# Optimization experiments

Measured on AMD Instinct MI355X. Metric: run time of the kernel, lower is better.

The kernel has to match this reference:

```python
import jax, jax.numpy as jnp
import numpy as np

NEG_SLOPE = 0.2

def _segment_softmax(logits, seg, num_segments):
    m = jax.ops.segment_max(logits, seg, num_segments=num_segments)
    m = jnp.where(jnp.isfinite(m), m, 0.0)
    e = jnp.exp(logits - m[seg])
    s = jax.ops.segment_sum(e, seg, num_segments=num_segments)
    return e / (s[seg] + 1e-16)

def _gat_conv(x, src, dst, W, att_src, att_dst, b):
    # PyG GATConv, heads=1, concat=True, add_self_loops=True
    N = x.shape[0]
    h = x @ W                                   # [N, C]
    a_src = h @ att_src                         # [N]
    a_dst = h @ att_dst                         # [N]
    loop = jnp.arange(N, dtype=src.dtype)
    s = jnp.concatenate([src, loop])            # add self-loops
    d = jnp.concatenate([dst, loop])
    logits = jax.nn.leaky_relu(a_src[s] + a_dst[d], NEG_SLOPE)  # [E+N]
    w = _segment_softmax(logits, d, N)
    out = jax.ops.segment_sum(h[s] * w[:, None], d, num_segments=N)
    return out + b

def _sage_conv(x, src, dst, W_l, W_r, b):
    # PyG SAGEConv, aggr='mean', root_weight=True, normalize=False
    N = x.shape[0]
    agg = jax.ops.segment_sum(x[src], dst, num_segments=N)      # [N, C]
    deg = jax.ops.segment_sum(jnp.ones_like(src, dtype=x.dtype), dst, num_segments=N)
    mean = agg / jnp.maximum(deg, 1.0)[:, None]
    return mean @ W_l + x @ W_r + b

def setup_inputs() -> dict:
    key = jax.random.key(0)
    ks = jax.random.split(key, 12)
    N, E, EL, F_IN, D = 100000, 1000000, 200000, 11, 64
    glorot = lambda k, sh: jax.random.uniform(k, sh, jnp.float32, -1.0, 1.0) * np.sqrt(6.0 / (sh[0] + sh[-1]))
    return {
        "x": jax.random.normal(ks[0], (N, F_IN), jnp.float32),
        "edge_index": jax.random.randint(ks[1], (2, E), 0, N, jnp.int64),
        "edge_label_index": jax.random.randint(ks[2], (2, EL), 0, N, jnp.int64),
        "W_gat": glorot(ks[3], (F_IN, D)),
        "att_src": glorot(ks[4], (D,)),
        "att_dst": glorot(ks[5], (D,)),
        "b_gat": jnp.zeros((D,), jnp.float32),
        "W1_l": glorot(ks[6], (D, D)),
        "W1_r": glorot(ks[7], (D, D)),
        "b1": jnp.zeros((D,), jnp.float32),
        "W2_l": glorot(ks[8], (D, D)),
        "W2_r": glorot(ks[9], (D, D)),
        "b2": jnp.zeros((D,), jnp.float32),
        "alpha": jnp.full((4,), 1.0 / 4.0, jnp.float32),  # num_layers + 1
    }

def reference(x, edge_index, edge_label_index, W_gat, att_src, att_dst, b_gat,
              W1_l, W1_r, b1, W2_l, W2_r, b2, alpha):
    src, dst = edge_index[0], edge_index[1]
    weights = jax.nn.softmax(alpha)
    # Faithful to original get_embedding (note: weights[1] is skipped, as in source)
    h = _gat_conv(x, src, dst, W_gat, att_src, att_dst, b_gat)
    out = h * weights[0]
    h = _sage_conv(h, src, dst, W1_l, W1_r, b1)
    out = out + h * weights[2]
    h = _sage_conv(h, src, dst, W2_l, W2_r, b2)
    out = out + h * weights[3]
    # link prediction: gather + elementwise dot
    return (out[edge_label_index[0]] * out[edge_label_index[1]]).sum(-1)
```

## Files before the change

kernel.cpp:

```cpp
#include <hip/hip_runtime.h>
#include <math.h>
#include <float.h>

#define NEG_SLOPE 0.2f
#define NCHUNK 128

typedef _Float16 half8 __attribute__((ext_vector_type(8)));
typedef float f32x4  __attribute__((ext_vector_type(4)));

__global__ __launch_bounds__(256) void gat_input_kernel(
    const float* __restrict__ x, const float* __restrict__ Wg,
    const float* __restrict__ att_src, const float* __restrict__ att_dst,
    _Float16* __restrict__ Hf, float* __restrict__ a_src, float* __restrict__ a_dst, int N,
    const float* __restrict__ W1l, const float* __restrict__ W1r,
    const float* __restrict__ W2l, const float* __restrict__ W2r,
    _Float16* __restrict__ W1hi, _Float16* __restrict__ W1lo,
    _Float16* __restrict__ W2hi, _Float16* __restrict__ W2lo,
    const float* __restrict__ alpha, float* __restrict__ wsm,
    _Float16* __restrict__ HG, _Float16* __restrict__ H1)
{
    if (blockIdx.x < 8) {
        if (blockIdx.x == 0 && threadIdx.x == 0) {
            float m = alpha[0];
            for (int i = 1; i < 4; i++) m = fmaxf(m, alpha[i]);
            float e[4], s = 0.f;
            for (int i = 0; i < 4; i++) { e[i] = expf(alpha[i] - m); s += e[i]; }
            for (int i = 0; i < 4; i++) wsm[i] = e[i] / s;
        }
        int which = blockIdx.x >> 2;
        const float* Wl = which ? W2l : W1l;
        const float* Wr = which ? W2r : W1r;
        _Float16* Whi = which ? W2hi : W1hi;
        _Float16* Wlo = which ? W2lo : W1lo;
        int idx = (blockIdx.x & 3) * 256 + threadIdx.x;
        int kc = idx >> 8, rem = idx & 255;
        int t = rem >> 6, ln = rem & 63;
        int quad = ln >> 4, col16 = ln & 15;
        int c = t * 16 + col16;
        #pragma unroll
        for (int j = 0; j < 8; j++) {
            int k = kc * 32 + quad * 8 + j;
            float w = (k < 64) ? Wl[k * 64 + c] : Wr[(k - 64) * 64 + c];
            _Float16 hi = (_Float16)w;
            _Float16 lo = (_Float16)(w - (float)hi);
            Whi[(size_t)idx * 8 + j] = hi;
            Wlo[(size_t)idx * 8 + j] = lo;
        }
    } else if (blockIdx.x == 8) {
        if (threadIdx.x < 64) Hf[(size_t)N * 64 + threadIdx.x] = (_Float16)0.f;
        else if (threadIdx.x < 128) HG[(size_t)N * 64 + (threadIdx.x - 64)] = (_Float16)0.f;
        else if (threadIdx.x < 192) H1[(size_t)N * 64 + (threadIdx.x - 128)] = (_Float16)0.f;
        else if (threadIdx.x == 192) a_src[N] = -1e30f;
    }
    __shared__ float Wl[11 * 64];
    int tid = threadIdx.x;
    for (int i = tid; i < 11 * 64; i += 256) Wl[i] = Wg[i];
    __syncthreads();
    int lane = tid & 63;
    int n = blockIdx.x * 4 + (tid >> 6);
    if (n >= N) return;
    float xv = (lane < 11) ? x[n * 11 + lane] : 0.f;
    float acc = 0.f;
    #pragma unroll
    for (int k = 0; k < 11; k++) acc += __shfl(xv, k, 64) * Wl[k * 64 + lane];
    Hf[(size_t)n * 64 + lane] = (_Float16)acc;
    float ps = acc * att_src[lane];
    float pd = acc * att_dst[lane];
    for (int off = 32; off; off >>= 1) {
        ps += __shfl_down(ps, off, 64);
        pd += __shfl_down(pd, off, 64);
    }
    if (lane == 0) { a_src[n] = ps; a_dst[n] = pd; }
}


__global__ __launch_bounds__(1024) void edge_hist_kernel(
    const int* __restrict__ dst, int* __restrict__ hist, int E, int NBK)
{
    __shared__ int c[1024];
    int t = threadIdx.x;
    c[t] = 0;
    __syncthreads();
    int chunk = (E + NCHUNK - 1) / NCHUNK;
    int lo = blockIdx.x * chunk;
    int hi = lo + chunk; if (hi > E) hi = E;
    for (int i = lo + t; i < hi; i += 1024)
        atomicAdd(&c[dst[i] >> 7], 1);
    __syncthreads();
    if (t < NBK) hist[t * NCHUNK + blockIdx.x] = c[t];
}

__global__ __launch_bounds__(1024) void edge_scatter_kernel(
    const int* __restrict__ src, const int* __restrict__ dst,
    const int* __restrict__ rstart, unsigned* __restrict__ ebuf, int E, int NBK)
{
    __shared__ int cur[1024];
    int t = threadIdx.x;
    if (t < NBK) cur[t] = rstart[t * NCHUNK + blockIdx.x];
    __syncthreads();
    int chunk = (E + NCHUNK - 1) / NCHUNK;
    int lo = blockIdx.x * chunk;
    int hi = lo + chunk; if (hi > E) hi = E;
    for (int i = lo + t; i < hi; i += 1024) {
        int d = dst[i];
        int p = atomicAdd(&cur[d >> 7], 1);
        ebuf[p] = ((unsigned)src[i] << 7) | (unsigned)(d & 127);
    }
}

__global__ __launch_bounds__(256) void scan_reduce_kernel(
    const int* __restrict__ v, int* __restrict__ bsum, int M)
{
    __shared__ int s[256];
    int t = threadIdx.x;
    int base = blockIdx.x * 1024 + t * 4;
    int sum = 0;
    #pragma unroll
    for (int j = 0; j < 4; j++) { int idx = base + j; if (idx < M) sum += v[idx]; }
    s[t] = sum; __syncthreads();
    for (int off = 128; off; off >>= 1) {
        if (t < off) s[t] += s[t + off];
        __syncthreads();
    }
    if (t == 0) bsum[blockIdx.x] = s[0];
}

__global__ __launch_bounds__(256) void scan_apply_kernel(
    const int* __restrict__ v, const int* __restrict__ bsum,
    int* __restrict__ out, int M, int NB)
{
    __shared__ int s[256];
    int t = threadIdx.x;
    int bv = (t < NB) ? bsum[t] : 0;
    s[t] = bv; __syncthreads();
    for (int off = 1; off < 256; off <<= 1) {
        int xx = (t >= off) ? s[t - off] : 0;
        __syncthreads();
        s[t] += xx;
        __syncthreads();
    }
    int blockoff = (blockIdx.x == 0) ? 0 : s[blockIdx.x - 1];
    __syncthreads();
    int base = blockIdx.x * 1024;
    int vv[4]; int sum = 0;
    #pragma unroll
    for (int j = 0; j < 4; j++) {
        int idx = base + t * 4 + j;
        vv[j] = (idx < M) ? v[idx] : 0;
        sum += vv[j];
    }
    s[t] = sum; __syncthreads();
    for (int off = 1; off < 256; off <<= 1) {
        int xx = (t >= off) ? s[t - off] : 0;
        __syncthreads();
        s[t] += xx;
        __syncthreads();
    }
    int ex = s[t] - sum + blockoff;
    #pragma unroll
    for (int j = 0; j < 4; j++) {
        int idx = base + t * 4 + j;
        if (idx < M) out[idx] = ex;
        ex += vv[j];
    }
}

__global__ __launch_bounds__(256) void bucket_build_kernel(
    const unsigned* __restrict__ ebuf, const int* __restrict__ rstart,
    int* __restrict__ cnt, int* __restrict__ rowstart,
    int* __restrict__ csr, int E, int N, int NBK)
{
    __shared__ int c[128];
    __shared__ int rs[128];
    __shared__ int cur[128];
    int b = blockIdx.x, t = threadIdx.x;
    if (t < 128) { c[t] = 0; cur[t] = 0; }
    __syncthreads();
    int beg = rstart[b * NCHUNK];
    int end = (b == NBK - 1) ? E : rstart[(b + 1) * NCHUNK];
    int n = end - beg;
    int pbeg = beg + 384 * b;
    for (int j = t; j < n; j += 256)
        atomicAdd(&c[ebuf[beg + j] & 127u], 1);
    __syncthreads();
    int myc = (t < 128) ? c[t] : 0;
    int mypc = (myc + 3) & ~3;
    if (t < 128) rs[t] = mypc;
    __syncthreads();
    for (int off = 1; off < 128; off <<= 1) {
        int v = (t < 128 && t >= off) ? rs[t - off] : 0;
        __syncthreads();
        if (t < 128) rs[t] += v;
        __syncthreads();
    }
    int ex = (t < 128) ? (rs[t] - mypc) : 0;
    __syncthreads();
    if (t < 128) rs[t] = ex;
    int base = b << 7;
    if (t < 128 && base + t < N) {
        cnt[base + t] = myc;
        rowstart[base + t] = pbeg + ex;
    }
    __syncthreads();
    for (int j = t; j < n; j += 256) {
        unsigned e = ebuf[beg + j];
        int d = (int)(e & 127u);
        int p = atomicAdd(&cur[d], 1);
        csr[pbeg + rs[d] + p] = (int)(e >> 7);
    }
    __syncthreads();
    if (t < 128) {
        for (int k = myc; k < mypc; k++) csr[pbeg + rs[t] + k] = N;
    }
}

__global__ __launch_bounds__(256) void gat_gather_kernel(
    const _Float16* __restrict__ Hf, const float* __restrict__ a_src,
    const float* __restrict__ a_dst, const float* __restrict__ bg,
    const int* __restrict__ rowstart, const int* __restrict__ cnt,
    const int* __restrict__ csr, const float* __restrict__ wsm,
    _Float16* __restrict__ HG, _Float16* __restrict__ outD, int N)
{
    const half8* __restrict__ H8 = (const half8*)Hf;
    int tid = threadIdx.x;
    int lane = tid & 63;
    int g = lane >> 3, sub = lane & 7;
    int gl = g << 3;
    int d = blockIdx.x * 32 + (tid >> 3);
    if (d >= N) return;
    float ad = a_dst[d];
    int beg = rowstart[d], deg = cnt[d];
    int degp = (deg + 3) & ~3;
    float a0 = a_src[d] + ad;
    float lg0 = a0 > 0.f ? a0 : NEG_SLOPE * a0;
    float w_self = expf(lg0);
    half8 hself = H8[(size_t)d * 8 + sub];
    float acc[8];
    #pragma unroll
    for (int c = 0; c < 8; c++) acc[c] = w_self * (float)hself[c];
    float l_lane = 0.f;
    for (int base = 0; base < degp; base += 8) {
        int nvc = degp - base; if (nvc > 8) nvc = 8;
        int sid = (sub < nvc) ? csr[beg + base + sub] : N;
        float aa = a_src[sid] + ad;
        float lgt = aa > 0.f ? aa : NEG_SLOPE * aa;
        float w = expf(lgt);
        l_lane += w;
        int ib[8]; float wb[8];
        #pragma unroll
        for (int j = 0; j < 8; j++) {
            ib[j] = __shfl(sid, gl + j, 64);
            wb[j] = __shfl(w, gl + j, 64);
        }
        half8 v[8];
        #pragma unroll
        for (int j = 0; j < 8; j++) v[j] = H8[(size_t)ib[j] * 8 + sub];
        #pragma unroll
        for (int j = 0; j < 8; j++) {
            #pragma unroll
            for (int c = 0; c < 8; c++) acc[c] += wb[j] * (float)v[j][c];
        }
    }
    #pragma unroll
    for (int off = 1; off < 8; off <<= 1) l_lane += __shfl_xor(l_lane, off, 64);
    float l = l_lane + w_self;
    float inv = 1.0f / (l + 1e-16f);
    float w0s = wsm[0];
    size_t idx = (size_t)d * 8 + sub;
    half8 hg, od;
    #pragma unroll
    for (int c = 0; c < 8; c++) {
        float o = acc[c] * inv + bg[sub * 8 + c];
        hg[c] = (_Float16)o;
        od[c] = (_Float16)(w0s * o);
    }
    ((half8*)HG)[idx] = hg;
    ((half8*)outD)[idx] = od;
}

__global__ __launch_bounds__(256) void sage_fused_kernel(
    const _Float16* __restrict__ Hin,
    const _Float16* __restrict__ Whi, const _Float16* __restrict__ Wlo,
    const float* __restrict__ bvec,
    const int* __restrict__ rowstart, const int* __restrict__ cnt,
    const int* __restrict__ csr, const float* __restrict__ wsm, int widx,
    _Float16* __restrict__ hout, _Float16* __restrict__ outD, int N)
{
    __shared__ __align__(16) char smem[64 * 68 * 4];
    float* Ot = (float*)smem;
    const half8* __restrict__ H8 = (const half8*)Hin;
    int tid = threadIdx.x;
    int lane = tid & 63;
    int nodeBase = blockIdx.x * 64;
    int sub = tid & 7;
    int g = lane >> 3;
    int gl = g << 3;

    #pragma unroll
    for (int pass = 0; pass < 2; pass++) {
        int dloc = pass * 32 + (tid >> 3);
        int d = nodeBase + dloc;
        float acc[8];
        #pragma unroll
        for (int c = 0; c < 8; c++) acc[c] = 0.f;
        half8 hself;
        #pragma unroll
        for (int c = 0; c < 8; c++) hself[c] = (_Float16)0.f;
        float invd = 0.f;
        if (d < N) {
            int beg = rowstart[d], deg = cnt[d];
            int degp = (deg + 3) & ~3;
            for (int base2 = 0; base2 < degp; base2 += 8) {
                int nvc = degp - base2; if (nvc > 8) nvc = 8;
                int sid = (sub < nvc) ? csr[beg + base2 + sub] : N;
                int ib[8];
                #pragma unroll
                for (int j = 0; j < 8; j++) ib[j] = __shfl(sid, gl + j, 64);
                half8 v[8];
                #pragma unroll
                for (int j = 0; j < 8; j++) v[j] = H8[(size_t)ib[j] * 8 + sub];
                #pragma unroll
                for (int j = 0; j < 8; j++) {
                    #pragma unroll
                    for (int c = 0; c < 8; c++) acc[c] += (float)v[j][c];
                }
            }
            invd = 1.0f / fmaxf((float)deg, 1.0f);
            hself = H8[(size_t)d * 8 + sub];
        }
        half8 ah;
        #pragma unroll
        for (int c = 0; c < 8; c++) ah[c] = (_Float16)(acc[c] * invd);
        int rbase = dloc * 256;
        int swz = (dloc & 7) << 4;
        *(half8*)(smem + ((rbase + sub * 16) ^ swz)) = ah;
        *(half8*)(smem + ((rbase + 128 + sub * 16) ^ swz)) = hself;
    }
    __syncthreads();

    int quad = lane >> 4, col16 = lane & 15;
    int wave = tid >> 6;
    int row = wave * 16 + col16;
    int rswz = (row & 7) << 4;
    f32x4 accq[4];
    #pragma unroll
    for (int t = 0; t < 4; t++) accq[t] = (f32x4){0.f, 0.f, 0.f, 0.f};
    #pragma unroll
    for (int kc = 0; kc < 4; kc++) {
        half8 a = *(const half8*)(smem + ((row * 256 + kc * 64 + quad * 16) ^ rswz));
        #pragma unroll
        for (int t = 0; t < 4; t++) {
            size_t off = (size_t)((kc * 4 + t) * 64 + lane) * 8;
            half8 bhi = *(const half8*)(Whi + off);
            half8 blo = *(const half8*)(Wlo + off);
            accq[t] = __builtin_amdgcn_mfma_f32_16x16x32_f16(a, bhi, accq[t], 0, 0, 0);
            accq[t] = __builtin_amdgcn_mfma_f32_16x16x32_f16(a, blo, accq[t], 0, 0, 0);
        }
    }
    __syncthreads();
    #pragma unroll
    for (int t = 0; t < 4; t++) {
        #pragma unroll
        for (int r = 0; r < 4; r++) {
            Ot[(wave * 16 + quad * 4 + r) * 68 + t * 16 + col16] = accq[t][r];
        }
    }
    __syncthreads();

    float w = wsm[widx];
    #pragma unroll
    for (int pass = 0; pass < 2; pass++) {
        int dloc = pass * 32 + (tid >> 3);
        int d = nodeBase + dloc;
        if (d >= N) continue;
        size_t idx = (size_t)d * 8 + sub;
        float4 o0 = *(float4*)&Ot[dloc * 68 + sub * 8];
        float4 o1 = *(float4*)&Ot[dloc * 68 + sub * 8 + 4];
        float4 b0 = *(const float4*)&bvec[sub * 8];
        float4 b1 = *(const float4*)&bvec[sub * 8 + 4];
        float o[8] = {o0.x + b0.x, o0.y + b0.y, o0.z + b0.z, o0.w + b0.w,
                      o1.x + b1.x, o1.y + b1.y, o1.z + b1.z, o1.w + b1.w};
        half8 od = ((half8*)outD)[idx];
        half8 ho;
        #pragma unroll
        for (int c = 0; c < 8; c++) {
            ho[c] = (_Float16)o[c];
            od[c] = (_Float16)((float)od[c] + w * o[c]);
        }
        if (hout) ((half8*)hout)[idx] = ho;
        ((half8*)outD)[idx] = od;
    }
}

__global__ __launch_bounds__(256) void link_pred_kernel(
    const int* __restrict__ eli, const _Float16* __restrict__ outf,
    float* __restrict__ out, int EL)
{
    const half8* __restrict__ o8 = (const half8*)outf;
    int e = blockIdx.x * 32 + (threadIdx.x >> 3);
    int sub = threadIdx.x & 7;
    if (e >= EL) return;
    int a = eli[e], b = eli[EL + e];
    half8 pa = o8[(size_t)a * 8 + sub];
    half8 pb = o8[(size_t)b * 8 + sub];
    float p = 0.f;
    #pragma unroll
    for (int c = 0; c < 8; c++) p += (float)pa[c] * (float)pb[c];
    for (int off = 4; off; off >>= 1) p += __shfl_xor(p, off, 64);
    if (sub == 0) out[e] = p;
}

extern "C" void kernel_launch(void* const* d_in, const int* in_sizes, int n_in,
                              void* d_out, int out_size, void* d_ws, size_t ws_size,
                              hipStream_t stream)
{
    const float* x      = (const float*)d_in[0];
    const int*   ei     = (const int*)d_in[1];
    const int*   eli    = (const int*)d_in[2];
    const float* Wg     = (const float*)d_in[3];
    const float* att_s  = (const float*)d_in[4];
    const float* att_d  = (const float*)d_in[5];
    const float* bg     = (const float*)d_in[6];
    const float* W1l    = (const float*)d_in[7];
    const float* W1r    = (const float*)d_in[8];
    const float* b1     = (const float*)d_in[9];
    const float* W2l    = (const float*)d_in[10];
    const float* W2r    = (const float*)d_in[11];
    const float* b2     = (const float*)d_in[12];
    const float* alpha  = (const float*)d_in[13];

    const int N  = in_sizes[0] / 11;
    const int E  = in_sizes[1] / 2;
    const int EL = in_sizes[2] / 2;
    const int NBK = (N + 127) >> 7;
    const int M   = NBK * NCHUNK;
    const int CSRSZ = E + 384 * NBK;

    const int* src = ei;
    const int* dst = ei + E;

    _Float16* Hf  = (_Float16*)d_ws;
    _Float16* HG  = Hf + (size_t)(N + 1) * 64;
    _Float16* H1  = HG + (size_t)(N + 1) * 64;
    _Float16* oD  = H1 + (size_t)(N + 1) * 64;
    _Float16* wf  = oD + (size_t)N * 64;
    _Float16* W1hi = wf;
    _Float16* W1lo = wf + 8192;
    _Float16* W2hi = wf + 16384;
    _Float16* W2lo = wf + 24576;
    float* wsm     = (float*)(wf + 32768);
    float* a_src   = wsm + 4;
    float* a_dst   = a_src + (N + 1);
    int*   cnt     = (int*)(a_dst + N);
    int*   rowstart= cnt + N;
    int*   hist    = rowstart + M ? rowstart + N : rowstart + N;
    int*   rstart  = hist + M;
    int*   bsum    = rstart + M;
    int*   csr     = bsum + 256;
    unsigned* ebuf = (unsigned*)H1;

    gat_input_kernel<<<(N + 3) / 4, 256, 0, stream>>>(x, Wg, att_s, att_d, Hf, a_src, a_dst, N,
                                                      W1l, W1r, W2l, W2r,
                                                      W1hi, W1lo, W2hi, W2lo, alpha, wsm,
                                                      HG, H1);

    edge_hist_kernel<<<NCHUNK, 1024, 0, stream>>>(dst, hist, E, NBK);
    int NB = (M + 1023) / 1024;
    scan_reduce_kernel<<<NB, 256, 0, stream>>>(hist, bsum, M);
    scan_apply_kernel<<<NB, 256, 0, stream>>>(hist, bsum, rstart, M, NB);
    edge_scatter_kernel<<<NCHUNK, 1024, 0, stream>>>(src, dst, rstart, ebuf, E, NBK);
    bucket_build_kernel<<<NBK, 256, 0, stream>>>(ebuf, rstart, cnt, rowstart, csr, E, N, NBK);

    gat_gather_kernel<<<(N + 31) / 32, 256, 0, stream>>>(Hf, a_src, a_dst, bg,
                                                         rowstart, cnt, csr, wsm, HG, oD, N);

    sage_fused_kernel<<<(N + 63) / 64, 256, 0, stream>>>(HG, W1hi, W1lo, b1,
                                                         rowstart, cnt, csr, wsm, 2, H1, oD, N);

    sage_fused_kernel<<<(N + 63) / 64, 256, 0, stream>>>(H1, W2hi, W2lo, b2,
                                                         rowstart, cnt, csr, wsm, 3, nullptr, oD, N);

    link_pred_kernel<<<(EL + 31) / 32, 256, 0, stream>>>(eli, oD, (float*)d_out, EL);
}
```

Before: 248.1 us.

## Fuse the whole GAT+SAGE pipeline into one cooperative persistent kernel

Replaces the chain of ten kernel launches with one cooperative persistent mega-kernel. Every stage (input projection, histogram, scan, scatter, bucket build, GAT gather, two SAGE layers, link prediction) runs as a grid-stride phase separated by grid.sync. The goal is to remove per-launch overhead and idle tails between small kernels. The cost is fewer blocks (bounded by occupancy, capped at 2048), smaller per-block thread counts for the histogram and scatter stages, and grid-wide barrier latency. The previous multi-kernel path remains as a fallback, and ebuf moves out of H1 into its own workspace region.

After: 260.3 us. 1.05x slower.

```diff
diff --git a/kernel.cpp b/kernel.cpp
--- a/kernel.cpp
+++ b/kernel.cpp
@@ -1,12 +1,439 @@
 #include <hip/hip_runtime.h>
+#include <hip/hip_cooperative_groups.h>
 #include <math.h>
 #include <float.h>
 
+namespace cg = cooperative_groups;
+
 #define NEG_SLOPE 0.2f
 #define NCHUNK 128
 
 typedef _Float16 half8 __attribute__((ext_vector_type(8)));
 typedef float f32x4  __attribute__((ext_vector_type(4)));
+
+struct MegaArgs {
+    const float *x, *Wg, *att_s, *att_d, *bg, *W1l, *W1r, *b1, *W2l, *W2r, *b2, *alpha;
+    const int *ei, *eli;
+    float *out;
+    _Float16 *Hf, *HG, *H1, *oD, *W1hi, *W1lo, *W2hi, *W2lo;
+    float *wsm, *a_src, *a_dst;
+    int *cnt, *rowstart, *hist, *rstart, *bsum, *csr;
+    unsigned *ebuf;
+    int N, E, EL, NBK, M, NB;
+};
+
+__device__ __forceinline__ void sage_layer_phase(
+    char* smem, const _Float16* __restrict__ Hin,
+    const _Float16* __restrict__ Whi, const _Float16* __restrict__ Wlo,
+    const float* __restrict__ bvec,
+    const int* __restrict__ rowstart, const int* __restrict__ cnt,
+    const int* __restrict__ csr, const float* __restrict__ wsm, int widx,
+    _Float16* __restrict__ hout, _Float16* __restrict__ outD, int N, int G)
+{
+    float* Ot = (float*)smem;
+    const half8* __restrict__ H8 = (const half8*)Hin;
+    int tid = threadIdx.x;
+    int lane = tid & 63;
+    int sub = tid & 7;
+    int g = lane >> 3;
+    int gl = g << 3;
+    int quad = lane >> 4, col16 = lane & 15;
+    int wave = tid >> 6;
+    int NGF = (N + 63) >> 6;
+    for (int vb = blockIdx.x; vb < NGF; vb += G) {
+        int nodeBase = vb * 64;
+        #pragma unroll
+        for (int pass = 0; pass < 2; pass++) {
+            int dloc = pass * 32 + (tid >> 3);
+            int d = nodeBase + dloc;
+            float acc[8];
+            #pragma unroll
+            for (int c = 0; c < 8; c++) acc[c] = 0.f;
+            half8 hself;
+            #pragma unroll
+            for (int c = 0; c < 8; c++) hself[c] = (_Float16)0.f;
+            float invd = 0.f;
+            if (d < N) {
+                int beg = rowstart[d], deg = cnt[d];
+                int degp = (deg + 3) & ~3;
+                for (int base2 = 0; base2 < degp; base2 += 8) {
+                    int nvc = degp - base2; if (nvc > 8) nvc = 8;
+                    int sid = (sub < nvc) ? csr[beg + base2 + sub] : N;
+                    int ib[8];
+                    #pragma unroll
+                    for (int j = 0; j < 8; j++) ib[j] = __shfl(sid, gl + j, 64);
+                    half8 v[8];
+                    #pragma unroll
+                    for (int j = 0; j < 8; j++) v[j] = H8[(size_t)ib[j] * 8 + sub];
+                    #pragma unroll
+                    for (int j = 0; j < 8; j++) {
+                        #pragma unroll
+                        for (int c = 0; c < 8; c++) acc[c] += (float)v[j][c];
+                    }
+                }
+                invd = 1.0f / fmaxf((float)deg, 1.0f);
+                hself = H8[(size_t)d * 8 + sub];
+            }
+            half8 ah;
+            #pragma unroll
+            for (int c = 0; c < 8; c++) ah[c] = (_Float16)(acc[c] * invd);
+            int rbase = dloc * 256;
+            int swz = (dloc & 7) << 4;
+            *(half8*)(smem + ((rbase + sub * 16) ^ swz)) = ah;
+            *(half8*)(smem + ((rbase + 128 + sub * 16) ^ swz)) = hself;
+        }
+        __syncthreads();
+        int row = wave * 16 + col16;
+        int rswz = (row & 7) << 4;
+        f32x4 accq[4];
+        #pragma unroll
+        for (int t = 0; t < 4; t++) accq[t] = (f32x4){0.f, 0.f, 0.f, 0.f};
+        #pragma unroll
+        for (int kc = 0; kc < 4; kc++) {
+            half8 av = *(const half8*)(smem + ((row * 256 + kc * 64 + quad * 16) ^ rswz));
+            #pragma unroll
+            for (int t = 0; t < 4; t++) {
+                size_t off = (size_t)((kc * 4 + t) * 64 + lane) * 8;
+                half8 bhi = *(const half8*)(Whi + off);
+                half8 blo = *(const half8*)(Wlo + off);
+                accq[t] = __builtin_amdgcn_mfma_f32_16x16x32_f16(av, bhi, accq[t], 0, 0, 0);
+                accq[t] = __builtin_amdgcn_mfma_f32_16x16x32_f16(av, blo, accq[t], 0, 0, 0);
+            }
+        }
+        __syncthreads();
+        #pragma unroll
+        for (int t = 0; t < 4; t++) {
+            #pragma unroll
+            for (int r = 0; r < 4; r++) {
+                Ot[(wave * 16 + quad * 4 + r) * 68 + t * 16 + col16] = accq[t][r];
+            }
+        }
+        __syncthreads();
+        float w = wsm[widx];
+        #pragma unroll
+        for (int pass = 0; pass < 2; pass++) {
+            int dloc = pass * 32 + (tid >> 3);
+            int d = nodeBase + dloc;
+            if (d < N) {
+                size_t idx = (size_t)d * 8 + sub;
+                float4 o0 = *(float4*)&Ot[dloc * 68 + sub * 8];
+                float4 o1 = *(float4*)&Ot[dloc * 68 + sub * 8 + 4];
+                float4 b0 = *(const float4*)&bvec[sub * 8];
+                float4 b1v = *(const float4*)&bvec[sub * 8 + 4];
+                float o[8] = {o0.x + b0.x, o0.y + b0.y, o0.z + b0.z, o0.w + b0.w,
+                              o1.x + b1v.x, o1.y + b1v.y, o1.z + b1v.z, o1.w + b1v.w};
+                half8 od = ((half8*)outD)[idx];
+                half8 ho;
+                #pragma unroll
+                for (int c = 0; c < 8; c++) {
+                    ho[c] = (_Float16)o[c];
+                    od[c] = (_Float16)((float)od[c] + w * o[c]);
+                }
+                if (hout) ((half8*)hout)[idx] = ho;
+                ((half8*)outD)[idx] = od;
+            }
+        }
+        __syncthreads();
+    }
+}
+
+__global__ __launch_bounds__(256) void mega_kernel(MegaArgs a)
+{
+    __shared__ __align__(16) char smem[64 * 68 * 4];
+    cg::grid_group grid = cg::this_grid();
+    const int tid = threadIdx.x;
+    const int G = (int)gridDim.x;
+    const int N = a.N, E = a.E, EL = a.EL, NBK = a.NBK, M = a.M, NB = a.NB;
+    const int* src = a.ei;
+    const int* dst = a.ei + E;
+
+    if (blockIdx.x < 8) {
+        if (blockIdx.x == 0 && tid == 0) {
+            float m = a.alpha[0];
+            for (int i = 1; i < 4; i++) m = fmaxf(m, a.alpha[i]);
+            float e[4], s = 0.f;
+            for (int i = 0; i < 4; i++) { e[i] = expf(a.alpha[i] - m); s += e[i]; }
+            for (int i = 0; i < 4; i++) a.wsm[i] = e[i] / s;
+        }
+        int which = (int)blockIdx.x >> 2;
+        const float* Wlp = which ? a.W2l : a.W1l;
+        const float* Wrp = which ? a.W2r : a.W1r;
+        _Float16* Whi = which ? a.W2hi : a.W1hi;
+        _Float16* Wlo = which ? a.W2lo : a.W1lo;
+        int idx = ((int)blockIdx.x & 3) * 256 + tid;
+        int kc = idx >> 8, rem = idx & 255;
+        int t = rem >> 6, ln = rem & 63;
+        int quad = ln >> 4, col16 = ln & 15;
+        int c = t * 16 + col16;
+        #pragma unroll
+        for (int j = 0; j < 8; j++) {
+            int k = kc * 32 + quad * 8 + j;
+            float w = (k < 64) ? Wlp[k * 64 + c] : Wrp[(k - 64) * 64 + c];
+            _Float16 hi = (_Float16)w;
+            _Float16 lo = (_Float16)(w - (float)hi);
+            Whi[(size_t)idx * 8 + j] = hi;
+            Wlo[(size_t)idx * 8 + j] = lo;
+        }
+    } else if (blockIdx.x == 8) {
+        if (tid < 64) a.Hf[(size_t)N * 64 + tid] = (_Float16)0.f;
+        else if (tid < 128) a.HG[(size_t)N * 64 + (tid - 64)] = (_Float16)0.f;
+        else if (tid < 192) a.H1[(size_t)N * 64 + (tid - 128)] = (_Float16)0.f;
+        else if (tid == 192) a.a_src[N] = -1e30f;
+    }
+    {
+        float* Wl = (float*)smem;
+        for (int i = tid; i < 11 * 64; i += 256) Wl[i] = a.Wg[i];
+        __syncthreads();
+        int lane = tid & 63, wv = tid >> 6;
+        int NG = (N + 3) >> 2;
+        for (int vb = blockIdx.x; vb < NG; vb += G) {
+            int n = vb * 4 + wv;
+            if (n < N) {
+                float xv = (lane < 11) ? a.x[n * 11 + lane] : 0.f;
+                float acc = 0.f;
+                #pragma unroll
+                for (int k = 0; k < 11; k++) acc += __shfl(xv, k, 64) * Wl[k * 64 + lane];
+                a.Hf[(size_t)n * 64 + lane] = (_Float16)acc;
+                float ps = acc * a.att_s[lane];
+                float pd = acc * a.att_d[lane];
+                for (int off = 32; off; off >>= 1) {
+                    ps += __shfl_down(ps, off, 64);
+                    pd += __shfl_down(pd, off, 64);
+                }
+                if (lane == 0) { a.a_src[n] = ps; a.a_dst[n] = pd; }
+            }
+        }
+    }
+    if ((int)blockIdx.x >= G - NCHUNK) {
+        int chunk = (int)blockIdx.x - (G - NCHUNK);
+        int* c = (int*)(smem + 4096);
+        for (int i = tid; i < 1024; i += 256) c[i] = 0;
+        __syncthreads();
+        int cs = (E + NCHUNK - 1) / NCHUNK;
+        int lo = chunk * cs;
+        int hi2 = lo + cs; if (hi2 > E) hi2 = E;
+        for (int i = lo + tid; i < hi2; i += 256)
+            atomicAdd(&c[dst[i] >> 7], 1);
+        __syncthreads();
+        for (int t = tid; t < NBK; t += 256) a.hist[t * NCHUNK + chunk] = c[t];
+    }
+    grid.sync();
+
+    {
+        int* s = (int*)smem;
+        for (int vb = blockIdx.x; vb < NB; vb += G) {
+            int base = vb * 1024 + tid * 4;
+            int sum = 0;
+            #pragma unroll
+            for (int j = 0; j < 4; j++) { int idx = base + j; if (idx < M) sum += a.hist[idx]; }
+            s[tid] = sum; __syncthreads();
+            for (int off = 128; off; off >>= 1) {
+                if (tid < off) s[tid] += s[tid + off];
+                __syncthreads();
+            }
+            if (tid == 0) a.bsum[vb] = s[0];
+            __syncthreads();
+        }
+    }
+    grid.sync();
+
+    {
+        int* s = (int*)smem;
+        for (int vb = blockIdx.x; vb < NB; vb += G) {
+            int bv = (tid < NB) ? a.bsum[tid] : 0;
+            s[tid] = bv; __syncthreads();
+            for (int off = 1; off < 256; off <<= 1) {
+                int xx = (tid >= off) ? s[tid - off] : 0;
+                __syncthreads();
+                s[tid] += xx;
+                __syncthreads();
+            }
+            int blockoff = (vb == 0) ? 0 : s[vb - 1];
+            __syncthreads();
+            int base = vb * 1024;
+            int vv[4]; int sum = 0;
+            #pragma unroll
+            for (int j = 0; j < 4; j++) {
+                int idx = base + tid * 4 + j;
+                vv[j] = (idx < M) ? a.hist[idx] : 0;
+                sum += vv[j];
+            }
+            s[tid] = sum; __syncthreads();
+            for (int off = 1; off < 256; off <<= 1) {
+                int xx = (tid >= off) ? s[tid - off] : 0;
+                __syncthreads();
+                s[tid] += xx;
+                __syncthreads();
+            }
+            int ex = s[tid] - sum + blockoff;
+            #pragma unroll
+            for (int j = 0; j < 4; j++) {
+                int idx = base + tid * 4 + j;
+                if (idx < M) a.rstart[idx] = ex;
+                ex += vv[j];
+            }
+            __syncthreads();
+        }
+    }
+    grid.sync();
+
+    {
+        int* cur = (int*)smem;
+        for (int chunk = blockIdx.x; chunk < NCHUNK; chunk += G) {
+            for (int t = tid; t < 1024; t += 256)
+                cur[t] = (t < NBK) ? a.rstart[t * NCHUNK + chunk] : 0;
+            __syncthreads();
+            int cs = (E + NCHUNK - 1) / NCHUNK;
+            int lo = chunk * cs;
+            int hi2 = lo + cs; if (hi2 > E) hi2 = E;
+            for (int i = lo + tid; i < hi2; i += 256) {
+                int d = dst[i];
+                int p = atomicAdd(&cur[d >> 7], 1);
+                a.ebuf[p] = ((unsigned)src[i] << 7) | (unsigned)(d & 127);
+            }
+            __syncthreads();
+        }
+    }
+    grid.sync();
+
+    {
+        int* c   = (int*)smem;
+        int* rs  = (int*)(smem + 512);
+        int* cur = (int*)(smem + 1024);
+        for (int b = blockIdx.x; b < NBK; b += G) {
+            if (tid < 128) { c[tid] = 0; cur[tid] = 0; }
+            __syncthreads();
+            int beg = a.rstart[b * NCHUNK];
+            int end = (b == NBK - 1) ? E : a.rstart[(b + 1) * NCHUNK];
+            int n = end - beg;
+            int pbeg = beg + 384 * b;
+            for (int j = tid; j < n; j += 256)
+                atomicAdd(&c[a.ebuf[beg + j] & 127u], 1);
+            __syncthreads();
+            int myc = (tid < 128) ? c[tid] : 0;
+            int mypc = (myc + 3) & ~3;
+            if (tid < 128) rs[tid] = mypc;
+            __syncthreads();
+            for (int off = 1; off < 128; off <<= 1) {
+                int v = (tid < 128 && tid >= off) ? rs[tid - off] : 0;
+                __syncthreads();
+                if (tid < 128) rs[tid] += v;
+                __syncthreads();
+            }
+            int ex = (tid < 128) ? (rs[tid] - mypc) : 0;
+            __syncthreads();
+            if (tid < 128) rs[tid] = ex;
+            int base = b << 7;
+            if (tid < 128 && base + tid < N) {
+                a.cnt[base + tid] = myc;
+                a.rowstart[base + tid] = pbeg + ex;
+            }
+            __syncthreads();
+            for (int j = tid; j < n; j += 256) {
+                unsigned e = a.ebuf[beg + j];
+                int d = (int)(e & 127u);
+                int p = atomicAdd(&cur[d], 1);
+                a.csr[pbeg + rs[d] + p] = (int)(e >> 7);
+            }
+            __syncthreads();
+            if (tid < 128) {
+                for (int k = myc; k < mypc; k++) a.csr[pbeg + rs[tid] + k] = N;
+            }
+            __syncthreads();
+        }
+    }
+    grid.sync();
+
+    {
+        const half8* __restrict__ H8 = (const half8*)a.Hf;
+        int lane = tid & 63;
+        int g = lane >> 3, sub = lane & 7;
+        int gl = g << 3;
+        int NV = (N + 31) >> 5;
+        for (int vb = blockIdx.x; vb < NV; vb += G) {
+            int d = vb * 32 + (tid >> 3);
+            if (d < N) {
+                float ad = a.a_dst[d];
+                int beg = a.rowstart[d], deg = a.cnt[d];
+                int degp = (deg + 3) & ~3;
+                float a0 = a.a_src[d] + ad;
+                float lg0 = a0 > 0.f ? a0 : NEG_SLOPE * a0;
+                float w_self = expf(lg0);
+                half8 hself = H8[(size_t)d * 8 + sub];
+                float acc[8];
+                #pragma unroll
+                for (int c = 0; c < 8; c++) acc[c] = w_self * (float)hself[c];
+                float l_lane = 0.f;
+                for (int base = 0; base < degp; base += 8) {
+                    int nvc = degp - base; if (nvc > 8) nvc = 8;
+                    int sid = (sub < nvc) ? a.csr[beg + base + sub] : N;
+                    float aa = a.a_src[sid] + ad;
+                    float lgt = aa > 0.f ? aa : NEG_SLOPE * aa;
+                    float w = expf(lgt);
+                    l_lane += w;
+                    int ib[8]; float wb[8];
+                    #pragma unroll
+                    for (int j = 0; j < 8; j++) {
+                        ib[j] = __shfl(sid, gl + j, 64);
+                        wb[j] = __shfl(w, gl + j, 64);
+                    }
+                    half8 v[8];
+                    #pragma unroll
+                    for (int j = 0; j < 8; j++) v[j] = H8[(size_t)ib[j] * 8 + sub];
+                    #pragma unroll
+                    for (int j = 0; j < 8; j++) {
+                        #pragma unroll
+                        for (int c = 0; c < 8; c++) acc[c] += wb[j] * (float)v[j][c];
+                    }
+                }
+                #pragma unroll
+                for (int off = 1; off < 8; off <<= 1) l_lane += __shfl_xor(l_lane, off, 64);
+                float l = l_lane + w_self;
+                float inv = 1.0f / (l + 1e-16f);
+                float w0s = a.wsm[0];
+                size_t idx = (size_t)d * 8 + sub;
+                half8 hg, od;
+                #pragma unroll
+                for (int c = 0; c < 8; c++) {
+                    float o = acc[c] * inv + a.bg[sub * 8 + c];
+                    hg[c] = (_Float16)o;
+                    od[c] = (_Float16)(w0s * o);
+                }
+                ((half8*)a.HG)[idx] = hg;
+                ((half8*)a.oD)[idx] = od;
+            }
+        }
+    }
+    grid.sync();
+
+    sage_layer_phase(smem, a.HG, a.W1hi, a.W1lo, a.b1,
+                     a.rowstart, a.cnt, a.csr, a.wsm, 2, a.H1, a.oD, N, G);
+    grid.sync();
+
+    sage_layer_phase(smem, a.H1, a.W2hi, a.W2lo, a.b2,
+                     a.rowstart, a.cnt, a.csr, a.wsm, 3, nullptr, a.oD, N, G);
+    grid.sync();
+
+    {
+        const half8* __restrict__ o8 = (const half8*)a.oD;
+        int NV = (EL + 31) >> 5;
+        int sub = tid & 7;
+        for (int vb = blockIdx.x; vb < NV; vb += G) {
+            int e = vb * 32 + (tid >> 3);
+            if (e < EL) {
+                int x0 = a.eli[e], x1 = a.eli[EL + e];
+                half8 pa = o8[(size_t)x0 * 8 + sub];
+                half8 pb = o8[(size_t)x1 * 8 + sub];
+                float p = 0.f;
+                #pragma unroll
+                for (int c = 0; c < 8; c++) p += (float)pa[c] * (float)pb[c];
+                for (int off = 4; off; off >>= 1) p += __shfl_xor(p, off, 64);
+                if (sub == 0) a.out[e] = p;
+            }
+        }
+    }
+}
+
 
 __global__ __launch_bounds__(256) void gat_input_kernel(
     const float* __restrict__ x, const float* __restrict__ Wg,
@@ -72,7 +499,6 @@
     }
     if (lane == 0) { a_src[n] = ps; a_dst[n] = pd; }
 }
-
 
 __global__ __launch_bounds__(1024) void edge_hist_kernel(
     const int* __restrict__ dst, int* __restrict__ hist, int E, int NBK)
@@ -287,109 +713,8 @@
     _Float16* __restrict__ hout, _Float16* __restrict__ outD, int N)
 {
     __shared__ __align__(16) char smem[64 * 68 * 4];
-    float* Ot = (float*)smem;
-    const half8* __restrict__ H8 = (const half8*)Hin;
-    int tid = threadIdx.x;
-    int lane = tid & 63;
-    int nodeBase = blockIdx.x * 64;
-    int sub = tid & 7;
-    int g = lane >> 3;
-    int gl = g << 3;
-
-    #pragma unroll
-    for (int pass = 0; pass < 2; pass++) {
-        int dloc = pass * 32 + (tid >> 3);
-        int d = nodeBase + dloc;
-        float acc[8];
-        #pragma unroll
-        for (int c = 0; c < 8; c++) acc[c] = 0.f;
-        half8 hself;
-        #pragma unroll
-        for (int c = 0; c < 8; c++) hself[c] = (_Float16)0.f;
-        float invd = 0.f;
-        if (d < N) {
-            int beg = rowstart[d], deg = cnt[d];
-            int degp = (deg + 3) & ~3;
-            for (int base2 = 0; base2 < degp; base2 += 8) {
-                int nvc = degp - base2; if (nvc > 8) nvc = 8;
-                int sid = (sub < nvc) ? csr[beg + base2 + sub] : N;
-                int ib[8];
-                #pragma unroll
-                for (int j = 0; j < 8; j++) ib[j] = __shfl(sid, gl + j, 64);
-                half8 v[8];
-                #pragma unroll
-                for (int j = 0; j < 8; j++) v[j] = H8[(size_t)ib[j] * 8 + sub];
-                #pragma unroll
-                for (int j = 0; j < 8; j++) {
-                    #pragma unroll
-                    for (int c = 0; c < 8; c++) acc[c] += (float)v[j][c];
-                }
-            }
-            invd = 1.0f / fmaxf((float)deg, 1.0f);
-            hself = H8[(size_t)d * 8 + sub];
-        }
-        half8 ah;
-        #pragma unroll
-        for (int c = 0; c < 8; c++) ah[c] = (_Float16)(acc[c] * invd);
-        int rbase = dloc * 256;
-        int swz = (dloc & 7) << 4;
-        *(half8*)(smem + ((rbase + sub * 16) ^ swz)) = ah;
-        *(half8*)(smem + ((rbase + 128 + sub * 16) ^ swz)) = hself;
-    }
-    __syncthreads();
-
-    int quad = lane >> 4, col16 = lane & 15;
-    int wave = tid >> 6;
-    int row = wave * 16 + col16;
-    int rswz = (row & 7) << 4;
-    f32x4 accq[4];
-    #pragma unroll
-    for (int t = 0; t < 4; t++) accq[t] = (f32x4){0.f, 0.f, 0.f, 0.f};
-    #pragma unroll
-    for (int kc = 0; kc < 4; kc++) {
-        half8 a = *(const half8*)(smem + ((row * 256 + kc * 64 + quad * 16) ^ rswz));
-        #pragma unroll
-        for (int t = 0; t < 4; t++) {
-            size_t off = (size_t)((kc * 4 + t) * 64 + lane) * 8;
-            half8 bhi = *(const half8*)(Whi + off);
-            half8 blo = *(const half8*)(Wlo + off);
-            accq[t] = __builtin_amdgcn_mfma_f32_16x16x32_f16(a, bhi, accq[t], 0, 0, 0);
-            accq[t] = __builtin_amdgcn_mfma_f32_16x16x32_f16(a, blo, accq[t], 0, 0, 0);
-        }
-    }
-    __syncthreads();
-    #pragma unroll
-    for (int t = 0; t < 4; t++) {
-        #pragma unroll
-        for (int r = 0; r < 4; r++) {
-            Ot[(wave * 16 + quad * 4 + r) * 68 + t * 16 + col16] = accq[t][r];
-        }
-    }
-    __syncthreads();
-
-    float w = wsm[widx];
-    #pragma unroll
-    for (int pass = 0; pass < 2; pass++) {
-        int dloc = pass * 32 + (tid >> 3);
-        int d = nodeBase + dloc;
-        if (d >= N) continue;
-        size_t idx = (size_t)d * 8 + sub;
-        float4 o0 = *(float4*)&Ot[dloc * 68 + sub * 8];
-        float4 o1 = *(float4*)&Ot[dloc * 68 + sub * 8 + 4];
-        float4 b0 = *(const float4*)&bvec[sub * 8];
-        float4 b1 = *(const float4*)&bvec[sub * 8 + 4];
-        float o[8] = {o0.x + b0.x, o0.y + b0.y, o0.z + b0.z, o0.w + b0.w,
-                      o1.x + b1.x, o1.y + b1.y, o1.z + b1.z, o1.w + b1.w};
-        half8 od = ((half8*)outD)[idx];
-        half8 ho;
-        #pragma unroll
-        for (int c = 0; c < 8; c++) {
-            ho[c] = (_Float16)o[c];
-            od[c] = (_Float16)((float)od[c] + w * o[c]);
-        }
-        if (hout) ((half8*)hout)[idx] = ho;
-        ((half8*)outD)[idx] = od;
-    }
+    sage_layer_phase(smem, Hin, Whi, Wlo, bvec, rowstart, cnt, csr, wsm, widx,
+                     hout, outD, N, (int)gridDim.x);
 }
 
 __global__ __launch_bounds__(256) void link_pred_kernel(
@@ -434,6 +759,7 @@
     const int EL = in_sizes[2] / 2;
     const int NBK = (N + 127) >> 7;
     const int M   = NBK * NCHUNK;
+    const int NB  = (M + 1023) / 1024;
     const int CSRSZ = E + 384 * NBK;
 
     const int* src = ei;
@@ -453,32 +779,62 @@
     float* a_dst   = a_src + (N + 1);
     int*   cnt     = (int*)(a_dst + N);
     int*   rowstart= cnt + N;
-    int*   hist    = rowstart + M ? rowstart + N : rowstart + N;
+    int*   hist    = rowstart + N;
     int*   rstart  = hist + M;
     int*   bsum    = rstart + M;
     int*   csr     = bsum + 256;
-    unsigned* ebuf = (unsigned*)H1;
-
-    gat_input_kernel<<<(N + 3) / 4, 256, 0, stream>>>(x, Wg, att_s, att_d, Hf, a_src, a_dst, N,
-                                                      W1l, W1r, W2l, W2r,
-                                                      W1hi, W1lo, W2hi, W2lo, alpha, wsm,
-                                                      HG, H1);
-
-    edge_hist_kernel<<<NCHUNK, 1024, 0, stream>>>(dst, hist, E, NBK);
-    int NB = (M + 1023) / 1024;
-    scan_reduce_kernel<<<NB, 256, 0, stream>>>(hist, bsum, M);
-    scan_apply_kernel<<<NB, 256, 0, stream>>>(hist, bsum, rstart, M, NB);
-    edge_scatter_kernel<<<NCHUNK, 1024, 0, stream>>>(src, dst, rstart, ebuf, E, NBK);
-    bucket_build_kernel<<<NBK, 256, 0, stream>>>(ebuf, rstart, cnt, rowstart, csr, E, N, NBK);
-
-    gat_gather_kernel<<<(N + 31) / 32, 256, 0, stream>>>(Hf, a_src, a_dst, bg,
-                                                         rowstart, cnt, csr, wsm, HG, oD, N);
-
-    sage_fused_kernel<<<(N + 63) / 64, 256, 0, stream>>>(HG, W1hi, W1lo, b1,
-                                                         rowstart, cnt, csr, wsm, 2, H1, oD, N);
-
-    sage_fused_kernel<<<(N + 63) / 64, 256, 0, stream>>>(H1, W2hi, W2lo, b2,
-                                                         rowstart, cnt, csr, wsm, 3, nullptr, oD, N);
-
-    link_pred_kernel<<<(EL + 31) / 32, 256, 0, stream>>>(eli, oD, (float*)d_out, EL);
-}
+    unsigned* ebuf = (unsigned*)(csr + CSRSZ);
+
+    static int s_maxB = -1;
+    if (s_maxB < 0) {
+        int mb = 0;
+        if (hipOccupancyMaxActiveBlocksPerMultiprocessor(&mb, mega_kernel, 256, 0)
+                != hipSuccess || mb < 1)
+            mb = 0;
+        s_maxB = mb;
+    }
+
+    bool coop_ok = false;
+    if (s_maxB >= 1) {
+        int G = s_maxB * 256;
+        if (G > 2048) G = 2048;
+        if (G < 256)  G = 256;
+        MegaArgs args;
+        args.x = x; args.Wg = Wg; args.att_s = att_s; args.att_d = att_d; args.bg = bg;
+        args.W1l = W1l; args.W1r = W1r; args.b1 = b1;
+        args.W2l = W2l; args.W2r = W2r; args.b2 = b2; args.alpha = alpha;
+        args.ei = ei; args.eli = eli; args.out = (float*)d_out;
+        args.Hf = Hf; args.HG = HG; args.H1 = H1; args.oD = oD;
+        args.W1hi = W1hi; args.W1lo = W1lo; args.W2hi = W2hi; args.W2lo = W2lo;
+        args.wsm = wsm; args.a_src = a_src; args.a_dst = a_dst;
+        args.cnt = cnt; args.rowstart = rowstart; args.hist = hist;
+        args.rstart = rstart; args.bsum = bsum; args.csr = csr; args.ebuf = ebuf;
+        args.N = N; args.E = E; args.EL = EL; args.NBK = NBK; args.M = M; args.NB = NB;
+        void* kp[] = { &args };
+        if (hipLaunchCooperativeKernel((const void*)mega_kernel, dim3(G), dim3(256),
+                                       kp, 0, stream) == hipSuccess)
+            coop_ok = true;
+        else
+            s_maxB = 0;
+    }
+
+    if (!coop_ok) {
+        gat_input_kernel<<<(N + 3) / 4, 256, 0, stream>>>(x, Wg, att_s, att_d, Hf,
+                                                          a_src, a_dst, N,
+                                                          W1l, W1r, W2l, W2r,
+                                                          W1hi, W1lo, W2hi, W2lo,
+                                                          alpha, wsm, HG, H1);
+        edge_hist_kernel<<<NCHUNK, 1024, 0, stream>>>(dst, hist, E, NBK);
+        scan_reduce_kernel<<<NB, 256, 0, stream>>>(hist, bsum, M);
+        scan_apply_kernel<<<NB, 256, 0, stream>>>(hist, bsum, rstart, M, NB);
+        edge_scatter_kernel<<<NCHUNK, 1024, 0, stream>>>(src, dst, rstart, ebuf, E, NBK);
+        bucket_build_kernel<<<NBK, 256, 0, stream>>>(ebuf, rstart, cnt, rowstart, csr, E, N, NBK);
+        gat_gather_kernel<<<(N + 31) / 32, 256, 0, stream>>>(Hf, a_src, a_dst, bg,
+                                                             rowstart, cnt, csr, wsm, HG, oD, N);
+        sage_fused_kernel<<<(N + 63) / 64, 256, 0, stream>>>(HG, W1hi, W1lo, b1,
+                                                             rowstart, cnt, csr, wsm, 2, H1, oD, N);
+        sage_fused_kernel<<<(N + 63) / 64, 256, 0, stream>>>(H1, W2hi, W2lo, b2,
+                                                             rowstart, cnt, csr, wsm, 3, nullptr, oD, N);
+        link_pred_kernel<<<(EL + 31) / 32, 256, 0, stream>>>(eli, oD, (float*)d_out, EL);
+    }
+}
```
